# Performance work log

Measured on AMD Instinct MI355X. Metric: run time of the kernel, lower is better.

Reference implementation:

```python
import jax, jax.numpy as jnp
import numpy as np

B, T, C = 2, 1024, 1024
H, D = 16, 64
E, I = 16, 256
EPS = 1e-5


def _ln(x, g, b):
    mu = x.mean(-1, keepdims=True)
    var = ((x - mu) ** 2).mean(-1, keepdims=True)
    return (x - mu) * jax.lax.rsqrt(var + EPS) * g + b


def setup_inputs() -> dict:
    key = jax.random.key(0)
    ks = jax.random.split(key, 10)
    s = 0.02
    return {
        "hidden_states": jax.random.normal(ks[0], (B, T, C), jnp.float32),
        "ln1_g": jnp.ones((C,), jnp.float32), "ln1_b": jnp.zeros((C,), jnp.float32),
        "ln2_g": jnp.ones((C,), jnp.float32), "ln2_b": jnp.zeros((C,), jnp.float32),
        "wq": jax.random.normal(ks[1], (C, C), jnp.float32) * s,
        "wk": jax.random.normal(ks[2], (C, C), jnp.float32) * s,
        "wv": jax.random.normal(ks[3], (C, C), jnp.float32) * s,
        "wo": jax.random.normal(ks[4], (C, C), jnp.float32) * s,
        "sim_matrix": jax.random.normal(ks[5], (C, E), jnp.float32),
        "threshold": jnp.zeros((1,), jnp.float32),
        "w1": jax.random.normal(ks[6], (E, C, I), jnp.float32) * s,
        "w2": jax.random.normal(ks[7], (E, I, C), jnp.float32) * s,
    }


def reference(hidden_states, ln1_g, ln1_b, ln2_g, ln2_b, wq, wk, wv, wo,
              sim_matrix, threshold, w1, w2):
    x = hidden_states
    # ---- attention (causal SDPA) ----
    h = _ln(x, ln1_g, ln1_b)
    q = (h @ wq).reshape(B, T, H, D)
    k = (h @ wk).reshape(B, T, H, D)
    v = (h @ wv).reshape(B, T, H, D)
    logits = jnp.einsum('bqhd,bkhd->bhqk', q, k) / np.float32(np.sqrt(D))
    causal = jnp.tril(jnp.ones((T, T), bool))
    logits = jnp.where(causal, logits, jnp.float32(-1e9))
    attn = jax.nn.softmax(logits, axis=-1)
    ao = jnp.einsum('bhqk,bkhd->bqhd', attn, v).reshape(B, T, C) @ wo
    x = x + ao
    # ---- MoE ----
    h2 = _ln(x, ln2_g, ln2_b).reshape(-1, C)          # [N, C]
    xn = h2 / jnp.linalg.norm(h2, axis=-1, keepdims=True)
    wn = sim_matrix / jnp.linalg.norm(sim_matrix, axis=0, keepdims=True)
    scores = xn @ wn                                   # [N, E]
    mask = scores > threshold                          # bool [N, E]
    k_per_token = mask.sum(-1)
    # dense expert compute; zero out non-activated slots (matches index_put buffer)
    mid = jax.nn.gelu(jnp.einsum('nc,eci->nei', h2, w1), approximate=False)
    expert_outputs_full = jnp.einsum('nei,eic->nec', mid, w2) * mask[:, :, None].astype(jnp.float32)
    # STE gate: value == mask, gradient flows to scores as identity
    ste = scores + jax.lax.stop_gradient(mask.astype(jnp.float32) - scores)
    final = (expert_outputs_full * ste[:, :, None]).sum(1).reshape(B, T, C)
    x = x + final
    return (x, scores, expert_outputs_full, k_per_token)
```

## Files before the change

kernel.cpp:

```cpp
#include <hip/hip_runtime.h>
#include <hip/hip_bf16.h>
#include <math.h>

#define BB 2
#define TT 1024
#define CC 1024
#define HH 16
#define DD 64
#define EE 16
#define II 256
#define NN (BB*TT)
#define EPSLN 1e-5f
#define LDA 72

typedef __attribute__((ext_vector_type(8))) short short8;
typedef __attribute__((ext_vector_type(4))) short s16x4;
typedef __attribute__((ext_vector_type(4))) float f32x4;

__device__ inline void splitbf(float x, short& hi, short& lo) {
    __hip_bfloat16 h = __float2bfloat16(x);
    float hf = __bfloat162float(h);
    __hip_bfloat16 l = __float2bfloat16(x - hf);
    hi = *(short*)&h;
    lo = *(short*)&l;
}

__global__ __launch_bounds__(256) void ln_kernel(const float* __restrict__ x,
                                                 const float* __restrict__ g,
                                                 const float* __restrict__ bta,
                                                 __hip_bfloat16* __restrict__ outh,
                                                 __hip_bfloat16* __restrict__ outl) {
    const int row = blockIdx.x, tid = threadIdx.x;
    __shared__ float r1[256], r2[256];
    const float* xr = x + (long)row * CC;
    float4 xv = ((const float4*)xr)[tid];
    float s  = xv.x + xv.y + xv.z + xv.w;
    float q2 = xv.x*xv.x + xv.y*xv.y + xv.z*xv.z + xv.w*xv.w;
    r1[tid] = s; r2[tid] = q2; __syncthreads();
    for (int st = 128; st > 0; st >>= 1) {
        if (tid < st) { r1[tid] += r1[tid+st]; r2[tid] += r2[tid+st]; }
        __syncthreads();
    }
    const float mu  = r1[0] * (1.f/CC);
    const float var = r2[0] * (1.f/CC) - mu*mu;
    const float rs  = rsqrtf(var + EPSLN);
    float4 gv = ((const float4*)g)[tid];
    float4 bv = ((const float4*)bta)[tid];
    float xs[4];
    xs[0] = (xv.x-mu)*rs*gv.x + bv.x;
    xs[1] = (xv.y-mu)*rs*gv.y + bv.y;
    xs[2] = (xv.z-mu)*rs*gv.z + bv.z;
    xs[3] = (xv.w-mu)*rs*gv.w + bv.w;
    s16x4 hv, lv;
    #pragma unroll
    for (int j = 0; j < 4; j++) { short h,l; splitbf(xs[j], h, l); hv[j]=h; lv[j]=l; }
    *(s16x4*)(outh + (long)row * CC + tid*4) = hv;
    *(s16x4*)(outl + (long)row * CC + tid*4) = lv;
}

__global__ __launch_bounds__(256) void ln2_router(const float* __restrict__ xio,
                                                  const float* __restrict__ g,
                                                  const float* __restrict__ bta,
                                                  const float* __restrict__ sim,
                                                  const float* __restrict__ cn,
                                                  const float* __restrict__ thr,
                                                  __hip_bfloat16* __restrict__ h2b,
                                                  float* __restrict__ scores,
                                                  float* __restrict__ kpt,
                                                  float* __restrict__ maskb,
                                                  int* __restrict__ cnt,
                                                  int* __restrict__ elist) {
    const int row = blockIdx.x, tid = threadIdx.x;
    __shared__ float r1[256], r2[256];
    __shared__ float red[256*17];
    float4 xv = ((const float4*)(xio + (long)row*CC))[tid];
    float s  = xv.x + xv.y + xv.z + xv.w;
    float q2 = xv.x*xv.x + xv.y*xv.y + xv.z*xv.z + xv.w*xv.w;
    r1[tid] = s; r2[tid] = q2; __syncthreads();
    for (int st = 128; st > 0; st >>= 1) {
        if (tid < st) { r1[tid] += r1[tid+st]; r2[tid] += r2[tid+st]; }
        __syncthreads();
    }
    const float mu  = r1[0] * (1.f/CC);
    const float var = r2[0] * (1.f/CC) - mu*mu;
    const float rs  = rsqrtf(var + EPSLN);
    float4 gv = ((const float4*)g)[tid];
    float4 bv = ((const float4*)bta)[tid];
    float ovs[4];
    ovs[0] = (xv.x-mu)*rs*gv.x + bv.x;
    ovs[1] = (xv.y-mu)*rs*gv.y + bv.y;
    ovs[2] = (xv.z-mu)*rs*gv.z + bv.z;
    ovs[3] = (xv.w-mu)*rs*gv.w + bv.w;
    {
        __hip_bfloat16* p = h2b + (long)row*CC + tid*4;
        p[0] = __float2bfloat16(ovs[0]); p[1] = __float2bfloat16(ovs[1]);
        p[2] = __float2bfloat16(ovs[2]); p[3] = __float2bfloat16(ovs[3]);
    }
    float acc[17] = {};
    #pragma unroll
    for (int j = 0; j < 4; j++) {
        const float v = ovs[j];
        acc[16] += v*v;
        const float* sr = sim + (long)(tid*4 + j)*EE;
        #pragma unroll
        for (int e2 = 0; e2 < EE; e2++) acc[e2] += v*sr[e2];
    }
    #pragma unroll
    for (int e2 = 0; e2 < 17; e2++) red[tid*17 + e2] = acc[e2];
    __syncthreads();
    for (int st = 128; st > 0; st >>= 1) {
        if (tid < st)
            for (int e2 = 0; e2 < 17; e2++) red[tid*17+e2] += red[(tid+st)*17+e2];
        __syncthreads();
    }
    if (tid < EE) {
        const float nrm = sqrtf(red[16]);
        const float sc  = red[tid] / (nrm * cn[tid]);
        scores[(long)row*EE + tid] = sc;
        const float mkv = sc > thr[0] ? 1.f : 0.f;
        maskb[(long)row*EE + tid] = mkv;
        red[tid] = mkv;
        if (mkv > 0.f) {
            int slot = atomicAdd(&cnt[tid], 1);
            elist[(long)tid*NN + slot] = row;
        }
    }
    __syncthreads();
    if (tid == 0) {
        float c2 = 0.f;
        for (int e2 = 0; e2 < EE; e2++) c2 += red[e2];
        kpt[row] = c2;
    }
}

__global__ __launch_bounds__(256) void transpose_split4(const float* __restrict__ W0,
                                                        const float* __restrict__ W1,
                                                        const float* __restrict__ W2,
                                                        const float* __restrict__ W3,
                                                        __hip_bfloat16* __restrict__ Wth_base,
                                                        __hip_bfloat16* __restrict__ Wtl_base) {
    const int z = blockIdx.z;
    const float* W = (z==0) ? W0 : (z==1) ? W1 : (z==2) ? W2 : W3;
    __hip_bfloat16* Wth = Wth_base + (long)z*CC*CC;
    __hip_bfloat16* Wtl = Wtl_base + (long)z*CC*CC;
    const int n0 = blockIdx.x * 32, k0 = blockIdx.y * 32;
    __shared__ float t[32][33];
    const int tx = threadIdx.x & 31, ty = threadIdx.x >> 5;
    #pragma unroll
    for (int i = 0; i < 4; i++)
        t[ty + i*8][tx] = W[(long)(k0 + ty + i*8)*CC + n0 + tx];
    __syncthreads();
    #pragma unroll
    for (int i = 0; i < 4; i++) {
        float v = t[tx][ty + i*8];
        short h, l; splitbf(v, h, l);
        *(short*)&Wth[(long)(n0 + ty + i*8)*CC + k0 + tx] = h;
        *(short*)&Wtl[(long)(n0 + ty + i*8)*CC + k0 + tx] = l;
    }
}

__global__ __launch_bounds__(256) void transpose_f2b_both(const float* __restrict__ w1,
                                                          const float* __restrict__ w2,
                                                          __hip_bfloat16* __restrict__ w1t,
                                                          __hip_bfloat16* __restrict__ w2t) {
    const int zz = blockIdx.z;
    const int half = zz >> 4, e = zz & 15;
    const float* W; __hip_bfloat16* Wt; int K, N, nbx;
    if (half == 0) { W = w1 + (long)e*CC*II; Wt = w1t + (long)e*CC*II; K = CC; N = II; nbx = II/32; }
    else           { W = w2 + (long)e*II*CC; Wt = w2t + (long)e*II*CC; K = II; N = CC; nbx = CC/32; }
    const int bx = blockIdx.x;
    const int n0 = (bx % nbx) * 32, k0 = (bx / nbx) * 32;
    __shared__ float t[32][33];
    const int tx = threadIdx.x & 31, ty = threadIdx.x >> 5;
    #pragma unroll
    for (int i = 0; i < 4; i++)
        t[ty + i*8][tx] = W[(long)(k0 + ty + i*8)*N + n0 + tx];
    __syncthreads();
    #pragma unroll
    for (int i = 0; i < 4; i++)
        Wt[(long)(n0 + ty + i*8)*K + k0 + tx] = __float2bfloat16(t[tx][ty + i*8]);
}

__global__ __launch_bounds__(256) void transpose_v_bf16(
        const __hip_bfloat16* __restrict__ Vh, const __hip_bfloat16* __restrict__ Vl,
        __hip_bfloat16* __restrict__ Vth, __hip_bfloat16* __restrict__ Vtl) {
    const int b = blockIdx.z;
    const int c0 = blockIdx.y * 32, t0 = blockIdx.x * 32;
    __shared__ unsigned short th[32][33], tl[32][33];
    const int tx = threadIdx.x & 31, ty = threadIdx.x >> 5;
    const unsigned short* vh = (const unsigned short*)Vh;
    const unsigned short* vl = (const unsigned short*)Vl;
    #pragma unroll
    for (int i = 0; i < 4; i++) {
        const long src = ((long)b*TT + t0 + ty + i*8)*CC + c0 + tx;
        th[ty + i*8][tx] = vh[src];
        tl[ty + i*8][tx] = vl[src];
    }
    __syncthreads();
    #pragma unroll
    for (int i = 0; i < 4; i++) {
        const int gc = c0 + ty + i*8;
        const int hh = gc >> 6, d = gc & 63;
        const long dst = ((long)(b*HH + hh)*64 + d)*TT + t0 + tx;
        ((unsigned short*)Vth)[dst] = th[tx][ty + i*8];
        ((unsigned short*)Vtl)[dst] = tl[tx][ty + i*8];
    }
}

__global__ __launch_bounds__(256, 2) void gemm_split_big(
        const __hip_bfloat16* __restrict__ Ah,
        const __hip_bfloat16* __restrict__ Al,
        const __hip_bfloat16* __restrict__ Bh_base,
        const __hip_bfloat16* __restrict__ Bl_base,
        __hip_bfloat16* __restrict__ Ch_base,
        __hip_bfloat16* __restrict__ Cl_base,
        int M, int N, int K) {
    __shared__ __hip_bfloat16 Ash[128][40], Asl[128][40];
    __shared__ __hip_bfloat16 Bsh[128][40], Bsl[128][40];
    const int z = blockIdx.z;
    const __hip_bfloat16* Bth = Bh_base + (long)z * N * K;
    const __hip_bfloat16* Btl = Bl_base + (long)z * N * K;
    const int n0 = blockIdx.x * 128, m0 = blockIdx.y * 128;
    const int tid = threadIdx.x;
    const int wave = tid >> 6, lane = tid & 63;
    const int wm = (wave >> 1) * 64, wn = (wave & 1) * 64;
    const int l15 = lane & 15, quad = lane >> 4;

    f32x4 acc[4][4] = {};

    for (int k0 = 0; k0 < K; k0 += 32) {
        #pragma unroll
        for (int it = 0; it < 2; it++) {
            const int idx = tid + it*256;
            const int r = idx >> 2, kg = (idx & 3) * 8;
            *(short8*)&Ash[r][kg] = *(const short8*)(Ah + (long)(m0 + r)*K + k0 + kg);
            *(short8*)&Asl[r][kg] = *(const short8*)(Al + (long)(m0 + r)*K + k0 + kg);
            *(short8*)&Bsh[r][kg] = *(const short8*)(Bth + (long)(n0 + r)*K + k0 + kg);
            *(short8*)&Bsl[r][kg] = *(const short8*)(Btl + (long)(n0 + r)*K + k0 + kg);
        }
        __syncthreads();
        short8 ah[4], al[4], bh[4], bl[4];
        #pragma unroll
        for (int i = 0; i < 4; i++) {
            ah[i] = *(const short8*)&Ash[wm + i*16 + l15][quad*8];
            al[i] = *(const short8*)&Asl[wm + i*16 + l15][quad*8];
            bh[i] = *(const short8*)&Bsh[wn + i*16 + l15][quad*8];
            bl[i] = *(const short8*)&Bsl[wn + i*16 + l15][quad*8];
        }
        #pragma unroll
        for (int mi = 0; mi < 4; mi++)
            #pragma unroll
            for (int ni = 0; ni < 4; ni++) {
                acc[mi][ni] = __builtin_amdgcn_mfma_f32_16x16x32_bf16(ah[mi], bh[ni], acc[mi][ni], 0,0,0);
                acc[mi][ni] = __builtin_amdgcn_mfma_f32_16x16x32_bf16(ah[mi], bl[ni], acc[mi][ni], 0,0,0);
                acc[mi][ni] = __builtin_amdgcn_mfma_f32_16x16x32_bf16(al[mi], bh[ni], acc[mi][ni], 0,0,0);
            }
        __syncthreads();
    }

    #pragma unroll
    for (int mi = 0; mi < 4; mi++)
        #pragma unroll
        for (int r = 0; r < 4; r++) {
            const int row = m0 + wm + mi*16 + quad*4 + r;
            #pragma unroll
            for (int ni = 0; ni < 4; ni++) {
                const int col = n0 + wn + ni*16 + l15;
                short hh, ll; splitbf(acc[mi][ni][r], hh, ll);
                *(short*)&Ch_base[(long)z*M*N + (long)row*N + col] = hh;
                *(short*)&Cl_base[(long)z*M*N + (long)row*N + col] = ll;
            }
        }
}

__global__ __launch_bounds__(256, 2) void gemm_split(
        const __hip_bfloat16* __restrict__ Ah,
        const __hip_bfloat16* __restrict__ Al,
        const __hip_bfloat16* __restrict__ Bth,
        const __hip_bfloat16* __restrict__ Btl,
        float* __restrict__ Cp,
        int M, int N, int K,
        const float* __restrict__ resid) {
    __shared__ __hip_bfloat16 Ash[64][40], Asl[64][40];
    __shared__ __hip_bfloat16 Bsh[128][40], Bsl[128][40];
    const int n0 = blockIdx.x * 128, m0 = blockIdx.y * 64;
    const int tid = threadIdx.x;
    const int wave = tid >> 6, lane = tid & 63;
    const int wm = (wave >> 1) * 32, wn = (wave & 1) * 64;
    const int l15 = lane & 15, quad = lane >> 4;

    f32x4 acc[2][4] = {};

    for (int k0 = 0; k0 < K; k0 += 32) {
        {
            const int r = tid >> 2, kg = (tid & 3) * 8;
            *(short8*)&Ash[r][kg] = *(const short8*)(Ah + (long)(m0 + r)*K + k0 + kg);
            *(short8*)&Asl[r][kg] = *(const short8*)(Al + (long)(m0 + r)*K + k0 + kg);
        }
        #pragma unroll
        for (int it = 0; it < 2; it++) {
            const int idx = tid + it*256;
            const int r = idx >> 2, kg = (idx & 3) * 8;
            *(short8*)&Bsh[r][kg] = *(const short8*)(Bth + (long)(n0 + r)*K + k0 + kg);
            *(short8*)&Bsl[r][kg] = *(const short8*)(Btl + (long)(n0 + r)*K + k0 + kg);
        }
        __syncthreads();
        short8 ah[2], al[2], bh[4], bl[4];
        #pragma unroll
        for (int mi = 0; mi < 2; mi++) {
            ah[mi] = *(const short8*)&Ash[wm + mi*16 + l15][quad*8];
            al[mi] = *(const short8*)&Asl[wm + mi*16 + l15][quad*8];
        }
        #pragma unroll
        for (int ni = 0; ni < 4; ni++) {
            bh[ni] = *(const short8*)&Bsh[wn + ni*16 + l15][quad*8];
            bl[ni] = *(const short8*)&Bsl[wn + ni*16 + l15][quad*8];
        }
        #pragma unroll
        for (int mi = 0; mi < 2; mi++)
            #pragma unroll
            for (int ni = 0; ni < 4; ni++) {
                acc[mi][ni] = __builtin_amdgcn_mfma_f32_16x16x32_bf16(ah[mi], bh[ni], acc[mi][ni], 0,0,0);
                acc[mi][ni] = __builtin_amdgcn_mfma_f32_16x16x32_bf16(ah[mi], bl[ni], acc[mi][ni], 0,0,0);
                acc[mi][ni] = __builtin_amdgcn_mfma_f32_16x16x32_bf16(al[mi], bh[ni], acc[mi][ni], 0,0,0);
            }
        __syncthreads();
    }

    #pragma unroll
    for (int mi = 0; mi < 2; mi++)
        #pragma unroll
        for (int r = 0; r < 4; r++) {
            const int row = m0 + wm + mi*16 + quad*4 + r;
            #pragma unroll
            for (int ni = 0; ni < 4; ni++) {
                const int col = n0 + wn + ni*16 + l15;
                Cp[(long)row*N + col] = acc[mi][ni][r] + resid[(long)row*N + col];
            }
        }
}

__global__ __launch_bounds__(256) void gemm_moe1_sparse(
        const __hip_bfloat16* __restrict__ A,
        const __hip_bfloat16* __restrict__ w1t,
        __hip_bfloat16* __restrict__ mid,
        const int* __restrict__ cnt,
        const int* __restrict__ elist) {
    constexpr int LDK = 40;
    __shared__ __hip_bfloat16 As[128][LDK];
    __shared__ __hip_bfloat16 Bs[128][LDK];
    __shared__ int rowmap[128];
    const int e = blockIdx.z;
    const int count = cnt[e];
    const int m0 = blockIdx.y * 128;
    if (m0 >= count) return;
    const int n0 = blockIdx.x * 128;
    const __hip_bfloat16* Bt = w1t + (long)e*II*CC;
    const int* lst = elist + (long)e*NN;
    const int tid = threadIdx.x;
    if (tid < 128) rowmap[tid] = lst[min(m0 + tid, count - 1)];
    __syncthreads();
    const int wave = tid >> 6, lane = tid & 63;
    const int wm = (wave >> 1) * 64, wn = (wave & 1) * 64;
    const int l15 = lane & 15, quad = lane >> 4;

    f32x4 acc[4][4] = {};

    for (int k0 = 0; k0 < CC; k0 += 32) {
        #pragma unroll
        for (int it = 0; it < 2; it++) {
            int idx = tid + it*256;
            int r = idx >> 2, kg = idx & 3;
            short8 av = *(const short8*)(A  + (long)rowmap[r]*CC + k0 + kg*8);
            short8 bv = *(const short8*)(Bt + (long)(n0 + r)*CC + k0 + kg*8);
            *(short8*)&As[r][kg*8] = av;
            *(short8*)&Bs[r][kg*8] = bv;
        }
        __syncthreads();
        short8 af[4], bff[4];
        #pragma unroll
        for (int i = 0; i < 4; i++) {
            af[i]  = *(const short8*)&As[wm + i*16 + l15][quad*8];
            bff[i] = *(const short8*)&Bs[wn + i*16 + l15][quad*8];
        }
        #pragma unroll
        for (int mi = 0; mi < 4; mi++)
            #pragma unroll
            for (int ni = 0; ni < 4; ni++)
                acc[mi][ni] = __builtin_amdgcn_mfma_f32_16x16x32_bf16(
                                  af[mi], bff[ni], acc[mi][ni], 0, 0, 0);
        __syncthreads();
    }

    #pragma unroll
    for (int mi = 0; mi < 4; mi++) {
        #pragma unroll
        for (int r = 0; r < 4; r++) {
            const int slot = m0 + wm + mi*16 + quad*4 + r;
            if (slot < count) {
                #pragma unroll
                for (int ni = 0; ni < 4; ni++) {
                    const int col = n0 + wn + ni*16 + l15;
                    float val = acc[mi][ni][r];
                    val = 0.5f*val*(1.f + erff(val*0.70710678118f));
                    mid[((long)e*NN + slot)*II + col] = __float2bfloat16(val);
                }
            }
        }
    }
}

__global__ __launch_bounds__(256) void gemm_moe2_sparse(
        const __hip_bfloat16* __restrict__ mid,
        const __hip_bfloat16* __restrict__ w2t,
        float* __restrict__ eo,
        const int* __restrict__ cnt,
        const int* __restrict__ elist) {
    constexpr int LDK = 40;
    __shared__ __hip_bfloat16 As[128][LDK];
    __shared__ __hip_bfloat16 Bs[128][LDK];
    __shared__ int rowmap[128];
    const int e = blockIdx.z;
    const int count = cnt[e];
    const int m0 = blockIdx.y * 128;
    if (m0 >= count) return;
    const int n0 = blockIdx.x * 128;
    const __hip_bfloat16* A  = mid + (long)e*NN*II;
    const __hip_bfloat16* Bt = w2t + (long)e*CC*II;
    const int* lst = elist + (long)e*NN;
    const int tid = threadIdx.x;
    if (tid < 128) rowmap[tid] = lst[min(m0 + tid, count - 1)];
    __syncthreads();
    const int wave = tid >> 6, lane = tid & 63;
    const int wm = (wave >> 1) * 64, wn = (wave & 1) * 64;
    const int l15 = lane & 15, quad = lane >> 4;

    f32x4 acc[4][4] = {};

    for (int k0 = 0; k0 < II; k0 += 32) {
        #pragma unroll
        for (int it = 0; it < 2; it++) {
            int idx = tid + it*256;
            int r = idx >> 2, kg = idx & 3;
            short8 av = *(const short8*)(A  + (long)(m0 + r)*II + k0 + kg*8);
            short8 bv = *(const short8*)(Bt + (long)(n0 + r)*II + k0 + kg*8);
            *(short8*)&As[r][kg*8] = av;
            *(short8*)&Bs[r][kg*8] = bv;
        }
        __syncthreads();
        short8 af[4], bff[4];
        #pragma unroll
        for (int i = 0; i < 4; i++) {
            af[i]  = *(const short8*)&As[wm + i*16 + l15][quad*8];
            bff[i] = *(const short8*)&Bs[wn + i*16 + l15][quad*8];
        }
        #pragma unroll
        for (int mi = 0; mi < 4; mi++)
            #pragma unroll
            for (int ni = 0; ni < 4; ni++)
                acc[mi][ni] = __builtin_amdgcn_mfma_f32_16x16x32_bf16(
                                  af[mi], bff[ni], acc[mi][ni], 0, 0, 0);
        __syncthreads();
    }

    #pragma unroll
    for (int mi = 0; mi < 4; mi++) {
        #pragma unroll
        for (int r = 0; r < 4; r++) {
            const int slot = m0 + wm + mi*16 + quad*4 + r;
            if (slot < count) {
                const int tok = rowmap[wm + mi*16 + quad*4 + r];
                #pragma unroll
                for (int ni = 0; ni < 4; ni++) {
                    const int col = n0 + wn + ni*16 + l15;
                    eo[((long)tok*EE + e)*CC + col] = acc[mi][ni][r];
                }
            }
        }
    }
}

__global__ __launch_bounds__(256) void eo_zero(const float* __restrict__ maskb,
                                               float* __restrict__ eo) {
    const int row = blockIdx.x, tid = threadIdx.x;
    const float4 z4 = {0.f, 0.f, 0.f, 0.f};
    #pragma unroll
    for (int e = 0; e < EE; e++) {
        if (maskb[(long)row*EE + e] == 0.f)
            ((float4*)(eo + ((long)row*EE + e)*CC))[tid] = z4;
    }
}

__global__ __launch_bounds__(256) void moe_sum_masked(const float* __restrict__ maskb,
                                                      const float* __restrict__ eo,
                                                      float* __restrict__ xio) {
    const int row = blockIdx.x, tid = threadIdx.x;
    float4 s = {0.f, 0.f, 0.f, 0.f};
    #pragma unroll
    for (int e = 0; e < EE; e++) {
        if (maskb[(long)row*EE + e] != 0.f) {
            float4 v = ((const float4*)(eo + ((long)row*EE + e)*CC))[tid];
            s.x += v.x; s.y += v.y; s.z += v.z; s.w += v.w;
        }
    }
    float4 xv = ((float4*)(xio + (long)row*CC))[tid];
    xv.x += s.x; xv.y += s.y; xv.z += s.z; xv.w += s.w;
    ((float4*)(xio + (long)row*CC))[tid] = xv;
}

__global__ __launch_bounds__(256, 4) void attn_split(
        const __hip_bfloat16* __restrict__ Qh, const __hip_bfloat16* __restrict__ Ql,
        const __hip_bfloat16* __restrict__ Kh, const __hip_bfloat16* __restrict__ Kl,
        const __hip_bfloat16* __restrict__ Vtg_h, const __hip_bfloat16* __restrict__ Vtg_l,
        float* __restrict__ Opart,
        float* __restrict__ mpart,
        float* __restrict__ lpart) {
    __shared__ __hip_bfloat16 KPh[64][LDA], KPl[64][LDA];
    __shared__ __hip_bfloat16 Vth[64][LDA], Vtl[64][LDA];

    const int bx = blockIdx.x;
    const int qt = 15 - (bx >> 1), half = bx & 1;
    const int h = blockIdx.y, b = blockIdx.z;
    const int tid = threadIdx.x;
    const int wave = tid >> 6, lane = tid & 63;
    const int l15 = lane & 15, quad = lane >> 4;
    const int wm = wave * 16;
    const long tbase = (long)b * TT * CC + (long)h * DD;
    const long vbase = (long)(b*HH + h) * 64 * TT;
    const int pidx = ((b*HH + h)*16 + qt)*2 + half;
    float* Op = Opart + (long)pidx * 4096;

    const int n_kt = qt + 1, mid_kt = (n_kt + 1) >> 1;
    const int kt_lo = half ? mid_kt : 0;
    const int kt_hi = half ? n_kt   : mid_kt;

    if (kt_lo >= kt_hi) {
        for (int i = tid; i < 64*64; i += 256) Op[i] = 0.f;
        if (tid < 64) { mpart[(long)pidx*64 + tid] = -1e30f; lpart[(long)pidx*64 + tid] = 0.f; }
        return;
    }

    short8 qh[2], ql[2];
    {
        const long qoff = tbase + (long)(qt*64 + wm + l15)*CC;
        #pragma unroll
        for (int kc = 0; kc < 2; kc++) {
            qh[kc] = *(const short8*)(Qh + qoff + kc*32 + quad*8);
            ql[kc] = *(const short8*)(Ql + qoff + kc*32 + quad*8);
        }
    }

    f32x4 oacc[4] = {};
    float m_run[4], l_run[4];
    #pragma unroll
    for (int r = 0; r < 4; r++) { m_run[r] = -1e30f; l_run[r] = 0.f; }

    for (int kt = kt_lo; kt < kt_hi; kt++) {
        __syncthreads();
        #pragma unroll
        for (int it = 0; it < 2; it++) {
            const int idx = tid + it*256;
            const int r = idx >> 3, g = (idx & 7)*8;
            const long koff = tbase + (long)(kt*64 + r)*CC + g;
            const long voff = vbase + (long)r*TT + kt*64 + g;
            *(short8*)&KPh[r][g] = *(const short8*)(Kh + koff);
            *(short8*)&KPl[r][g] = *(const short8*)(Kl + koff);
            *(short8*)&Vth[r][g] = *(const short8*)(Vtg_h + voff);
            *(short8*)&Vtl[r][g] = *(const short8*)(Vtg_l + voff);
        }
        __syncthreads();

        f32x4 s[4] = {};
        #pragma unroll
        for (int nt = 0; nt < 4; nt++)
            #pragma unroll
            for (int kc = 0; kc < 2; kc++) {
                short8 bh = *(const short8*)&KPh[nt*16 + l15][kc*32 + quad*8];
                short8 bl = *(const short8*)&KPl[nt*16 + l15][kc*32 + quad*8];
                s[nt] = __builtin_amdgcn_mfma_f32_16x16x32_bf16(qh[kc], bh, s[nt], 0,0,0);
                s[nt] = __builtin_amdgcn_mfma_f32_16x16x32_bf16(qh[kc], bl, s[nt], 0,0,0);
                s[nt] = __builtin_amdgcn_mfma_f32_16x16x32_bf16(ql[kc], bh, s[nt], 0,0,0);
            }

        const bool diag = (kt == qt);
        float alpha[4];
        float pr[4][4];
        #pragma unroll
        for (int r = 0; r < 4; r++) {
            const int rowg = wm + quad*4 + r;
            float sv[4], mx = -1e30f;
            #pragma unroll
            for (int nt = 0; nt < 4; nt++) {
                float val = s[nt][r] * 0.125f;
                if (diag && (nt*16 + l15) > rowg) val = -1e30f;
                sv[nt] = val;
                mx = fmaxf(mx, val);
            }
            #pragma unroll
            for (int off = 1; off < 16; off <<= 1) mx = fmaxf(mx, __shfl_xor(mx, off, 16));
            const float mnew = fmaxf(m_run[r], mx);
            alpha[r] = __expf(m_run[r] - mnew);
            float rs = 0.f;
            #pragma unroll
            for (int nt = 0; nt < 4; nt++) {
                float p = __expf(sv[nt] - mnew);
                pr[r][nt] = p;
                rs += p;
            }
            #pragma unroll
            for (int off = 1; off < 16; off <<= 1) rs += __shfl_xor(rs, off, 16);
            l_run[r] = l_run[r]*alpha[r] + rs;
            m_run[r] = mnew;
        }
        __syncthreads();

        #pragma unroll
        for (int r = 0; r < 4; r++)
            #pragma unroll
            for (int nt = 0; nt < 4; nt++) {
                short hh, ll; splitbf(pr[r][nt], hh, ll);
                *(short*)&KPh[wm + quad*4 + r][nt*16 + l15] = hh;
                *(short*)&KPl[wm + quad*4 + r][nt*16 + l15] = ll;
            }

        #pragma unroll
        for (int dt = 0; dt < 4; dt++)
            #pragma unroll
            for (int r = 0; r < 4; r++)
                oacc[dt][r] *= alpha[r];
        #pragma unroll
        for (int kc = 0; kc < 2; kc++) {
            short8 ph = *(const short8*)&KPh[wm + l15][kc*32 + quad*8];
            short8 pl = *(const short8*)&KPl[wm + l15][kc*32 + quad*8];
            #pragma unroll
            for (int dt = 0; dt < 4; dt++) {
                short8 vh = *(const short8*)&Vth[dt*16 + l15][kc*32 + quad*8];
                short8 vl = *(const short8*)&Vtl[dt*16 + l15][kc*32 + quad*8];
                oacc[dt] = __builtin_amdgcn_mfma_f32_16x16x32_bf16(ph, vh, oacc[dt], 0,0,0);
                oacc[dt] = __builtin_amdgcn_mfma_f32_16x16x32_bf16(ph, vl, oacc[dt], 0,0,0);
                oacc[dt] = __builtin_amdgcn_mfma_f32_16x16x32_bf16(pl, vh, oacc[dt], 0,0,0);
            }
        }
    }

    #pragma unroll
    for (int dt = 0; dt < 4; dt++)
        #pragma unroll
        for (int r = 0; r < 4; r++)
            Op[(wm + quad*4 + r)*64 + dt*16 + l15] = oacc[dt][r];
    if (l15 == 0) {
        #pragma unroll
        for (int r = 0; r < 4; r++) {
            mpart[(long)pidx*64 + wm + quad*4 + r] = m_run[r];
            lpart[(long)pidx*64 + wm + quad*4 + r] = l_run[r];
        }
    }
}

__global__ __launch_bounds__(256) void attn_merge(const float* __restrict__ Opart,
                                                  const float* __restrict__ mpart,
                                                  const float* __restrict__ lpart,
                                                  __hip_bfloat16* __restrict__ aoh,
                                                  __hip_bfloat16* __restrict__ aol) {
    const int qt = blockIdx.x, h = blockIdx.y, b = blockIdx.z;
    const int pA = ((b*HH + h)*16 + qt)*2, pB = pA + 1;
    const int tid = threadIdx.x;
    const int r = tid >> 2, c0 = (tid & 3) * 16;
    const float mA = mpart[(long)pA*64 + r], mB = mpart[(long)pB*64 + r];
    const float lA = lpart[(long)pA*64 + r], lB = lpart[(long)pB*64 + r];
    const float M  = fmaxf(mA, mB);
    const float wA = __expf(mA - M), wB = __expf(mB - M);
    const float inv = 1.f / (lA*wA + lB*wB);
    const float* OA = Opart + (long)pA*4096 + r*64 + c0;
    const float* OB = Opart + (long)pB*4096 + r*64 + c0;
    const long dst = (long)b*TT*CC + (long)(qt*64 + r)*CC + h*DD + c0;
    #pragma unroll
    for (int j = 0; j < 16; j += 4) {
        float4 oa = *(const float4*)(OA + j);
        float4 ob = *(const float4*)(OB + j);
        float xs[4];
        xs[0] = (oa.x*wA + ob.x*wB)*inv;
        xs[1] = (oa.y*wA + ob.y*wB)*inv;
        xs[2] = (oa.z*wA + ob.z*wB)*inv;
        xs[3] = (oa.w*wA + ob.w*wB)*inv;
        s16x4 hv, lv;
        #pragma unroll
        for (int t = 0; t < 4; t++) { short hh,ll; splitbf(xs[t],hh,ll); hv[t]=hh; lv[t]=ll; }
        *(s16x4*)(aoh + dst + j) = hv;
        *(s16x4*)(aol + dst + j) = lv;
    }
}

__global__ __launch_bounds__(256) void colnorm_kernel(const float* __restrict__ sim,
                                                      float* __restrict__ cn,
                                                      int* __restrict__ cnt) {
    const int e = blockIdx.x, tid = threadIdx.x;
    __shared__ float red[256];
    float s = 0.f;
    for (int c = tid; c < CC; c += 256) {
        float vv = sim[(long)c*EE + e];
        s += vv*vv;
    }
    red[tid] = s; __syncthreads();
    for (int st = 128; st > 0; st >>= 1) {
        if (tid < st) red[tid] += red[tid+st];
        __syncthreads();
    }
    if (tid == 0) { cn[e] = sqrtf(red[0]); cnt[e] = 0; }
}

extern "C" void kernel_launch(void* const* d_in, const int* in_sizes, int n_in,
                              void* d_out, int out_size, void* d_ws, size_t ws_size,
                              hipStream_t stream) {
    const float* x     = (const float*)d_in[0];
    const float* ln1_g = (const float*)d_in[1];
    const float* ln1_b = (const float*)d_in[2];
    const float* ln2_g = (const float*)d_in[3];
    const float* ln2_b = (const float*)d_in[4];
    const float* wq    = (const float*)d_in[5];
    const float* wk    = (const float*)d_in[6];
    const float* wv    = (const float*)d_in[7];
    const float* wo    = (const float*)d_in[8];
    const float* sim   = (const float*)d_in[9];
    const float* thr   = (const float*)d_in[10];
    const float* w1    = (const float*)d_in[11];
    const float* w2    = (const float*)d_in[12];

    float* out_x      = (float*)d_out;
    float* out_scores = out_x + (long)NN*CC;
    float* out_eo     = out_scores + (long)NN*EE;
    float* out_kpt    = out_eo + (long)NN*EE*CC;

    const long MF = (long)NN*CC;
    const long CK = (long)CC*CC;
    float* ws   = (float*)d_ws;
    __hip_bfloat16* aoh = (__hip_bfloat16*)ws;
    __hip_bfloat16* aol = (__hip_bfloat16*)(ws + MF/2);
    __hip_bfloat16* qkvh = (__hip_bfloat16*)(ws + MF);
    __hip_bfloat16* qkvl = (__hip_bfloat16*)(ws + MF + 3*MF/2);
    __hip_bfloat16* vth = (__hip_bfloat16*)(ws + 4*MF);
    __hip_bfloat16* vtl = (__hip_bfloat16*)(ws + 4*MF + MF/2);
    __hip_bfloat16* h2b = (__hip_bfloat16*)(ws + 5*MF);
    float* Opart = ws + 5*MF + MF/2;
    __hip_bfloat16* hh  = (__hip_bfloat16*)(ws + 5*MF + MF/2);
    __hip_bfloat16* hl  = (__hip_bfloat16*)(ws + 6*MF);
    __hip_bfloat16* mid = (__hip_bfloat16*)(ws + 5*MF + MF/2);
    __hip_bfloat16* wsph = (__hip_bfloat16*)(ws + 7*MF + MF/2);
    __hip_bfloat16* wspl = (__hip_bfloat16*)(ws + 8*MF + MF/2);
    __hip_bfloat16* w1t  = (__hip_bfloat16*)(ws + 7*MF + MF/2);
    __hip_bfloat16* w2t  = (__hip_bfloat16*)(ws + 8*MF + MF/2);
    float* maskb = ws + 9*MF + MF/2;
    float* cn    = maskb + (long)NN*EE;
    float* mpart = cn + 16;
    float* lpart = mpart + 1024L*64;
    int*   cnt   = (int*)(lpart + 1024L*64);
    int*   elist = cnt + 16;

    colnorm_kernel<<<EE, 256, 0, stream>>>(sim, cn, cnt);

    {
        dim3 gt(CC/32, CC/32, 4);
        transpose_split4<<<gt, 256, 0, stream>>>(wq, wk, wv, wo, wsph, wspl);
    }

    ln_kernel<<<NN, 256, 0, stream>>>(x, ln1_g, ln1_b, hh, hl);

    {
        dim3 gq(CC/128, NN/128, 3);
        gemm_split_big<<<gq, 256, 0, stream>>>(hh, hl, wsph, wspl,
                                               qkvh, qkvl, NN, CC, CC);
    }

    {
        dim3 gv(TT/32, CC/32, BB);
        transpose_v_bf16<<<gv, 256, 0, stream>>>(qkvh + 2*(long)NN*CC, qkvl + 2*(long)NN*CC,
                                                 vth, vtl);
    }

    {
        dim3 gattn(32, HH, BB);
        attn_split<<<gattn, 256, 0, stream>>>(qkvh, qkvl,
                                              qkvh + (long)NN*CC, qkvl + (long)NN*CC,
                                              vth, vtl, Opart, mpart, lpart);
        dim3 gmerge(16, HH, BB);
        attn_merge<<<gmerge, 256, 0, stream>>>(Opart, mpart, lpart, aoh, aol);
    }

    {
        dim3 go(CC/128, NN/64, 1);
        gemm_split<<<go, 256, 0, stream>>>(aoh, aol, wsph + 3*CK, wspl + 3*CK,
                                           out_x, NN, CC, CC, x);
    }

    {
        dim3 ge(256, 1, 2*EE);
        transpose_f2b_both<<<ge, 256, 0, stream>>>(w1, w2, w1t, w2t);
    }

    ln2_router<<<NN, 256, 0, stream>>>(out_x, ln2_g, ln2_b, sim, cn, thr,
                                       h2b, out_scores, out_kpt, maskb,
                                       cnt, elist);

    eo_zero<<<NN, 256, 0, stream>>>(maskb, out_eo);

    {
        dim3 g(II/128, NN/128, EE);
        gemm_moe1_sparse<<<g, 256, 0, stream>>>(h2b, w1t, mid, cnt, elist);
    }

    {
        dim3 g(CC/128, NN/128, EE);
        gemm_moe2_sparse<<<g, 256, 0, stream>>>(mid, w2t, out_eo, cnt, elist);
    }

    moe_sum_masked<<<NN, 256, 0, stream>>>(maskb, out_eo, out_x);
}
```

Before: 470.0 us.

## Use direct global-to-LDS loads in split GEMM and fuse expert-output zeroing

The big split-bf16 GEMM now stages A/B tiles with global_load_lds 16-byte transfers straight into LDS instead of going through registers, and drops the LDS row padding to fit the required contiguous layout. The separate eo_zero kernel is folded into the final masked-sum kernel, which zeroes the inactive expert slots while accumulating the active ones. This aims to cut register staging overhead and one kernel launch. Removing the padding may add LDS bank conflicts on the fragment reads.

Result: faster. 458.7 us (-2.4%).

```diff
diff --git a/kernel.cpp b/kernel.cpp
--- a/kernel.cpp
+++ b/kernel.cpp
@@ -16,6 +16,10 @@
 typedef __attribute__((ext_vector_type(8))) short short8;
 typedef __attribute__((ext_vector_type(4))) short s16x4;
 typedef __attribute__((ext_vector_type(4))) float f32x4;
+
+#define GLOAD_LDS16(g, l) \
+    __builtin_amdgcn_global_load_lds((const __attribute__((address_space(1))) void*)(g), \
+                                     (__attribute__((address_space(3))) void*)(l), 16, 0, 0)
 
 __device__ inline void splitbf(float x, short& hi, short& lo) {
     __hip_bfloat16 h = __float2bfloat16(x);
@@ -215,8 +219,8 @@
         __hip_bfloat16* __restrict__ Ch_base,
         __hip_bfloat16* __restrict__ Cl_base,
         int M, int N, int K) {
-    __shared__ __hip_bfloat16 Ash[128][40], Asl[128][40];
-    __shared__ __hip_bfloat16 Bsh[128][40], Bsl[128][40];
+    __shared__ __hip_bfloat16 Ash[128][32], Asl[128][32];
+    __shared__ __hip_bfloat16 Bsh[128][32], Bsl[128][32];
     const int z = blockIdx.z;
     const __hip_bfloat16* Bth = Bh_base + (long)z * N * K;
     const __hip_bfloat16* Btl = Bl_base + (long)z * N * K;
@@ -230,13 +234,16 @@
 
     for (int k0 = 0; k0 < K; k0 += 32) {
         #pragma unroll
-        for (int it = 0; it < 2; it++) {
-            const int idx = tid + it*256;
-            const int r = idx >> 2, kg = (idx & 3) * 8;
-            *(short8*)&Ash[r][kg] = *(const short8*)(Ah + (long)(m0 + r)*K + k0 + kg);
-            *(short8*)&Asl[r][kg] = *(const short8*)(Al + (long)(m0 + r)*K + k0 + kg);
-            *(short8*)&Bsh[r][kg] = *(const short8*)(Bth + (long)(n0 + r)*K + k0 + kg);
-            *(short8*)&Bsl[r][kg] = *(const short8*)(Btl + (long)(n0 + r)*K + k0 + kg);
+        for (int i = 0; i < 2; i++) {
+            const int chunk = wave*2 + i;
+            const int r = chunk*16 + (lane >> 2);
+            const int c8 = (lane & 3) * 8;
+            const long aoff = (long)(m0 + r)*K + k0 + c8;
+            const long boff = (long)(n0 + r)*K + k0 + c8;
+            GLOAD_LDS16(Ah  + aoff, &Ash[chunk*16][0]);
+            GLOAD_LDS16(Al  + aoff, &Asl[chunk*16][0]);
+            GLOAD_LDS16(Bth + boff, &Bsh[chunk*16][0]);
+            GLOAD_LDS16(Btl + boff, &Bsl[chunk*16][0]);
         }
         __syncthreads();
         short8 ah[4], al[4], bh[4], bl[4];
@@ -480,27 +487,20 @@
     }
 }
 
-__global__ __launch_bounds__(256) void eo_zero(const float* __restrict__ maskb,
-                                               float* __restrict__ eo) {
-    const int row = blockIdx.x, tid = threadIdx.x;
-    const float4 z4 = {0.f, 0.f, 0.f, 0.f};
-    #pragma unroll
-    for (int e = 0; e < EE; e++) {
-        if (maskb[(long)row*EE + e] == 0.f)
-            ((float4*)(eo + ((long)row*EE + e)*CC))[tid] = z4;
-    }
-}
-
-__global__ __launch_bounds__(256) void moe_sum_masked(const float* __restrict__ maskb,
-                                                      const float* __restrict__ eo,
-                                                      float* __restrict__ xio) {
+__global__ __launch_bounds__(256) void moe_sum_zero(const float* __restrict__ maskb,
+                                                    float* __restrict__ eo,
+                                                    float* __restrict__ xio) {
     const int row = blockIdx.x, tid = threadIdx.x;
     float4 s = {0.f, 0.f, 0.f, 0.f};
+    const float4 z4 = {0.f, 0.f, 0.f, 0.f};
     #pragma unroll
     for (int e = 0; e < EE; e++) {
+        float4* p = ((float4*)(eo + ((long)row*EE + e)*CC)) + tid;
         if (maskb[(long)row*EE + e] != 0.f) {
-            float4 v = ((const float4*)(eo + ((long)row*EE + e)*CC))[tid];
+            float4 v = *p;
             s.x += v.x; s.y += v.y; s.z += v.z; s.w += v.w;
+        } else {
+            *p = z4;
         }
     }
     float4 xv = ((float4*)(xio + (long)row*CC))[tid];
@@ -801,8 +801,6 @@
                                        h2b, out_scores, out_kpt, maskb,
                                        cnt, elist);
 
-    eo_zero<<<NN, 256, 0, stream>>>(maskb, out_eo);
-
     {
         dim3 g(II/128, NN/128, EE);
         gemm_moe1_sparse<<<g, 256, 0, stream>>>(h2b, w1t, mid, cnt, elist);
@@ -813,5 +811,5 @@
         gemm_moe2_sparse<<<g, 256, 0, stream>>>(mid, w2t, out_eo, cnt, elist);
     }
 
-    moe_sum_masked<<<NN, 256, 0, stream>>>(maskb, out_eo, out_x);
-}
+    moe_sum_zero<<<NN, 256, 0, stream>>>(maskb, out_eo, out_x);
+}
```
